# Kernel optimization log

Hardware: AMD Instinct MI355X
Metric: run time of the kernel (lower is better)

## Reference

```python
import jax, jax.numpy as jnp
import numpy as np

N = 100000
E = 1600000
F_IN = 256
H1, C1 = 4, 32          # layer 1: heads=4, out_channels=32, concat=True -> 128
H2, C2 = 1, 16          # layer 2: heads=1, out_channels=nclass=16, concat=False
SLOPE = 0.2             # leaky relu negative slope


def setup_inputs() -> dict:
    key = jax.random.key(0)
    ks = jax.random.split(key, 10)
    x = jax.random.normal(ks[0], (N, F_IN), dtype=jnp.float32)
    row = jax.random.randint(ks[1], (E,), 0, N, dtype=jnp.int32)      # source j
    off = jax.random.randint(ks[2], (E,), 1, N, dtype=jnp.int32)
    col = ((row + off) % N).astype(jnp.int32)                          # target i, no self loops
    edge_index = jnp.stack([row, col])

    def glorot(k, shape, fan_in, fan_out):
        lim = np.sqrt(6.0 / (fan_in + fan_out))
        return jax.random.uniform(k, shape, jnp.float32, -lim, lim)

    W1 = glorot(ks[3], (F_IN, H1 * C1), F_IN, H1 * C1)
    att1 = glorot(ks[4], (1, H1, 2 * C1), H1, 2 * C1)
    b1 = jnp.zeros((H1 * C1,), jnp.float32)
    W2 = glorot(ks[5], (H1 * C1, H2 * C2), H1 * C1, H2 * C2)
    att2 = glorot(ks[6], (1, H2, 2 * C2), H2, 2 * C2)
    b2 = jnp.zeros((C2,), jnp.float32)
    return {"x": x, "edge_index": edge_index, "W1": W1, "att1": att1,
            "b1": b1, "W2": W2, "att2": att2, "b2": b2}


def gcn_norm(edge_index, num_nodes):
    # add_remaining_self_loops + symmetric normalization (GeoLayer.norm)
    loop = jnp.arange(num_nodes, dtype=edge_index.dtype)
    row = jnp.concatenate([edge_index[0], loop])
    col = jnp.concatenate([edge_index[1], loop])
    w = jnp.ones(row.shape[0], jnp.float32)
    deg = jax.ops.segment_sum(w, row, num_segments=num_nodes)
    dinv = jnp.where(deg > 0, jax.lax.rsqrt(deg), 0.0)
    return row, col, dinv[row] * w * dinv[col]


def segment_softmax(alpha, seg, num_segments):
    amax = jax.ops.segment_max(alpha, seg, num_segments=num_segments)
    ex = jnp.exp(alpha - amax[seg])
    denom = jax.ops.segment_sum(ex, seg, num_segments=num_segments)
    return ex / (denom[seg] + 1e-16)


def geo_layer(x, row, col, ew, W, att, b, heads, out_ch, concat):
    n = x.shape[0]
    xt = (x @ W).reshape(n, heads, out_ch)
    x_i = xt[col]                         # [E+N, H, C] target features
    x_j = xt[row]                         # [E+N, H, C] source features
    wl, wr = att[:, :, :out_ch], att[:, :, out_ch:]
    # (cat([x_i,x_j],-1) * att).sum(-1) == (x_i*wl).sum + (x_j*wr).sum
    alpha = (x_i * wl).sum(-1) + (x_j * wr).sum(-1)     # [E+N, H]
    alpha = jnp.where(alpha >= 0, alpha, SLOPE * alpha)  # leaky_relu
    alpha = segment_softmax(alpha, col, n)
    msg = ew[:, None, None] * x_j * alpha[:, :, None]    # [E+N, H, C]
    out = jax.ops.segment_sum(msg, col, num_segments=n)  # scatter-add to targets
    out = out.reshape(n, heads * out_ch) if concat else out.mean(axis=1)
    return out + b


def reference(x, edge_index, W1, att1, b1, W2, att2, b2):
    # norm is identical for both layers (edge_weight=None each time)
    row, col, ew = gcn_norm(edge_index, x.shape[0])
    h = geo_layer(x, row, col, ew, W1, att1, b1, H1, C1, True)
    h = jax.nn.relu(h)
    out = geo_layer(h, row, col, ew, W2, att2, b2, H2, C2, False)
    return out
```

## Files before the change

kernel.cpp:

```cpp
#include <hip/hip_runtime.h>
#include <math.h>

#define TPB 256
#define SEGN 512
#define SCAP 14336
#define CHB 8192
#define CAPC 12288

__device__ __forceinline__ float lrelu(float a){ return a >= 0.f ? a : 0.2f*a; }

typedef __attribute__((ext_vector_type(8))) short bf16x8;
typedef __attribute__((ext_vector_type(4))) float f32x4;

__device__ __forceinline__ unsigned short bfr(float f){
  unsigned u = __float_as_uint(f);
  return (unsigned short)((u + 0x7fffu + ((u >> 16) & 1u)) >> 16);
}

__device__ __forceinline__ void gl_lds16(const void* g, void* l){
  __builtin_amdgcn_global_load_lds(
      (const __attribute__((address_space(1))) void*)g,
      (__attribute__((address_space(3))) void*)l, 16, 0, 0);
}


__global__ __launch_bounds__(256) void k_bucketM(const int* __restrict__ rows, const int* __restrict__ cols,
    int* __restrict__ bcurC, int* __restrict__ bcurR,
    unsigned* __restrict__ ebufC, unsigned short* __restrict__ ebufR, int E, int NSEG2){
  __shared__ int lhC[256], lbC[256], lhR[256], lbR[256];
  int tid = threadIdx.x;
  int e0 = blockIdx.x * CHB;
  #pragma unroll 1
  for(int r=0; r<4; r++){
    lhC[tid] = 0; lhR[tid] = 0;
    __syncthreads();
    int eb = e0 + r*2048;
    unsigned pk[8]; int sgC[8], rkC[8], sgR[8], rkR[8]; int pvR[8];
    #pragma unroll
    for(int i=0;i<8;i++){
      int e = eb + i*256 + tid;
      sgC[i] = -1;
      if(e < E){
        int cc = cols[e], rr = rows[e];
        sgC[i] = cc >> 9;
        pk[i]  = ((unsigned)(cc & (SEGN-1)) << 17) | (unsigned)rr;
        rkC[i] = atomicAdd(&lhC[sgC[i]], 1);
        sgR[i] = rr >> 9;
        pvR[i] = rr & (SEGN-1);
        rkR[i] = atomicAdd(&lhR[sgR[i]], 1);
      }
    }
    __syncthreads();
    if(tid < NSEG2){
      int c = lhC[tid];  lbC[tid] = c  ? atomicAdd(&bcurC[tid], c)  : 0;
      int c2 = lhR[tid]; lbR[tid] = c2 ? atomicAdd(&bcurR[tid], c2) : 0;
    }
    __syncthreads();
    #pragma unroll
    for(int i=0;i<8;i++)
      if(sgC[i] >= 0){
        int p = lbC[sgC[i]] + rkC[i];
        if(p < CAPC) ebufC[sgC[i]*CAPC + p] = pk[i];
        int p2 = lbR[sgR[i]] + rkR[i];
        if(p2 < CAPC) ebufR[sgR[i]*CAPC + p2] = (unsigned short)pvR[i];
      }
    __syncthreads();
  }
}

__global__ __launch_bounds__(256) void k_cntseg(const int* __restrict__ bcurC, const int* __restrict__ bcurR,
    const unsigned* __restrict__ ebufC, const unsigned short* __restrict__ ebufR,
    int* __restrict__ cnt, float* __restrict__ dinv, int* __restrict__ bsum, int N){
  __shared__ int hc[SEGN];
  __shared__ int hr[SEGN];
  __shared__ int red[256];
  int s = blockIdx.x, tid = threadIdx.x;
  int lo = s*SEGN;
  int nn = min(SEGN, N - lo);
  for(int i=tid; i<SEGN; i+=256){ hc[i] = 0; hr[i] = 0; }
  __syncthreads();
  int cb = s*CAPC;
  int cc = min(bcurC[s], CAPC);
  int rc = min(bcurR[s], CAPC);
  for(int j=tid; j<cc; j+=256) atomicAdd(&hc[ebufC[cb + j] >> 17], 1);
  for(int j=tid; j<rc; j+=256) atomicAdd(&hr[ebufR[cb + j]], 1);
  __syncthreads();
  int tsum = 0;
  for(int i=tid; i<nn; i+=256){
    int c = hc[i] + 1;
    cnt[lo+i]  = c;
    tsum += c;
    dinv[lo+i] = 1.f / sqrtf((float)(hr[i] + 1));
  }
  red[tid] = tsum; __syncthreads();
  for(int off=128; off>0; off>>=1){
    if(tid < off) red[tid] += red[tid+off];
    __syncthreads();
  }
  if(tid == 0) bsum[s] = red[0];
}

__global__ void k_scan_bsum(int* bsum, int NB){
  __shared__ int s[256];
  int t = threadIdx.x;
  int v = (t < NB) ? bsum[t] : 0;
  s[t] = v; __syncthreads();
  for(int off=1; off<256; off<<=1){
    int add = (t >= off) ? s[t-off] : 0;
    __syncthreads();
    s[t] += add;
    __syncthreads();
  }
  if(t < NB) bsum[t] = s[t] - v;
}

__global__ __launch_bounds__(256) void k_sortfill2(const int* __restrict__ cnt,
    const int* __restrict__ bsum, const int* __restrict__ bcurC,
    const unsigned* __restrict__ ebuf, int* __restrict__ offs,
    int* __restrict__ csr, int N){
  __shared__ int lcur[SEGN];
  __shared__ int lbuf[SCAP];
  __shared__ int sdata[256];
  int s = blockIdx.x, tid = threadIdx.x;
  int lo = s*SEGN;
  int nn = min(SEGN, N - lo);
  int base = bsum[s];
  int i0 = tid*2, i1 = i0+1;
  int v0 = (i0 < nn) ? cnt[lo+i0] : 0;
  int v1 = (i1 < nn) ? cnt[lo+i1] : 0;
  int ssum = v0 + v1;
  sdata[tid] = ssum; __syncthreads();
  int mine = ssum;
  for(int off=1; off<256; off<<=1){
    int add = (tid >= off) ? sdata[tid-off] : 0;
    __syncthreads();
    sdata[tid] += add;
    __syncthreads();
  }
  int total = sdata[255];
  int run0 = sdata[tid] - mine;
  int run1 = run0 + v0;
  int eb = s*CAPC;
  int ec = min(bcurC[s], CAPC);
  if(total <= SCAP){
    if(i0 < nn){
      offs[lo+i0] = base + run0;
      lbuf[run0]  = lo + i0;
      lcur[i0]    = run0 + 1;
      if(lo+i0 == N-1) offs[N] = base + run0 + v0;
    }
    if(i1 < nn){
      offs[lo+i1] = base + run1;
      lbuf[run1]  = lo + i1;
      lcur[i1]    = run1 + 1;
      if(lo+i1 == N-1) offs[N] = base + run1 + v1;
    }
    __syncthreads();
    for(int j=tid; j<ec; j+=256){
      unsigned pk = ebuf[eb + j];
      int li  = pk >> 17;
      int row = pk & 0x1FFFF;
      int p = atomicAdd(&lcur[li], 1);
      lbuf[p] = row;
    }
    __syncthreads();
    for(int j=tid; j<total; j+=256) csr[base + j] = lbuf[j];
  } else {
    if(i0 < nn){
      offs[lo+i0] = base + run0;
      csr[base+run0] = lo + i0;
      lcur[i0] = base + run0 + 1;
      if(lo+i0 == N-1) offs[N] = base + run0 + v0;
    }
    if(i1 < nn){
      offs[lo+i1] = base + run1;
      csr[base+run1] = lo + i1;
      lcur[i1] = base + run1 + 1;
      if(lo+i1 == N-1) offs[N] = base + run1 + v1;
    }
    __syncthreads();
    for(int j=tid; j<ec; j+=256){
      unsigned pk = ebuf[eb + j];
      int li  = pk >> 17;
      int row = pk & 0x1FFFF;
      int p = atomicAdd(&lcur[li], 1);
      csr[p] = row;
    }
  }
}


__global__ void k_prepW(const float* __restrict__ W, short* __restrict__ Whi,
                        short* __restrict__ Wlo){
  int idx = blockIdx.x*256 + threadIdx.x;
  int n = idx >> 8, k = idx & 255;
  float f = W[k*128 + n];
  unsigned short h = bfr(f);
  float hf = __uint_as_float(((unsigned)h) << 16);
  Whi[n*256 + k] = (short)h;
  Wlo[n*256 + k] = (short)bfr(f - hf);
}


#define BUFB 24576
__global__ __launch_bounds__(256) void k_gemm1(
    const float* __restrict__ x,
    const short* __restrict__ Whi, const short* __restrict__ Wlo,
    const float* __restrict__ att1,
    unsigned* __restrict__ xtb, float* __restrict__ sl, float* __restrict__ sr, int N){
  __shared__ __align__(16) char smem[2*BUFB];
  float* fx = (float*)smem;
  float* att_sh = (float*)(smem + 17408);

  int tid = threadIdx.x;
  int n0 = blockIdx.x * 64;
  int w = tid >> 6, l = tid & 63;
  int wm = w & 1, wn = w >> 1;
  int lm = l & 15, lq = l >> 4;

  f32x4 acc[2][4];
  #pragma unroll
  for(int a=0;a<2;a++)
    #pragma unroll
    for(int b=0;b<4;b++) acc[a][b] = (f32x4){0.f,0.f,0.f,0.f};

  int ua0 = (w<<6) | l, ua1 = 256 + ua0;
  int ar0 = ua0 >> 3, as0 = (ua0 & 7) ^ (ar0 & 7);
  int ar1 = ua1 >> 3, as1 = (ua1 & 7) ^ (ar1 & 7);
  const float* gA0 = x + (size_t)min(n0 + ar0, N-1)*256 + as0*4;
  const float* gA1 = x + (size_t)min(n0 + ar1, N-1)*256 + as1*4;
  int ub0 = (w<<6) | l,  ub1 = 256 + ub0;
  int br0 = ub0 >> 2, bs0 = (ub0 & 3) ^ ((br0 >> 1) & 3);
  int br1 = ub1 >> 2, bs1 = (ub1 & 3) ^ ((br1 >> 1) & 3);
  const short* gBh0 = Whi + br0*256 + bs0*8;
  const short* gBh1 = Whi + br1*256 + bs1*8;
  const short* gBl0 = Wlo + br0*256 + bs0*8;
  const short* gBl1 = Wlo + br1*256 + bs1*8;
  int woff = w << 10;

  int offAf[2][2], offB[4];
  #pragma unroll
  for(int mt=0;mt<2;mt++){
    int rr = wm*32 + mt*16 + lm;
    offAf[mt][0] = rr*32 + (((2*lq+0) ^ (rr&7)) << 2);
    offAf[mt][1] = rr*32 + (((2*lq+1) ^ (rr&7)) << 2);
  }
  #pragma unroll
  for(int nt=0;nt<4;nt++){
    int rr = wn*64 + nt*16 + lm;
    offB[nt] = rr*32 + ((lq ^ ((rr>>1)&3)) << 3);
  }

  {
    char* base = smem;
    gl_lds16(gA0,  base          + woff);
    gl_lds16(gA1,  base + 4096   + woff);
    gl_lds16(gBh0, base + 8192   + woff);
    gl_lds16(gBh1, base + 12288  + woff);
    gl_lds16(gBl0, base + 16384  + woff);
    gl_lds16(gBl1, base + 20480  + woff);
  }
  __syncthreads();

  int cur = 0;
  #pragma unroll 1
  for(int c=0;c<8;c++){
    if(c < 7){
      int kf = (c+1) << 5;
      char* base = smem + (cur^1)*BUFB;
      gl_lds16(gA0  + kf, base          + woff);
      gl_lds16(gA1  + kf, base + 4096   + woff);
      gl_lds16(gBh0 + kf, base + 8192   + woff);
      gl_lds16(gBh1 + kf, base + 12288  + woff);
      gl_lds16(gBl0 + kf, base + 16384  + woff);
      gl_lds16(gBl1 + kf, base + 20480  + woff);
    }
    float* Axf = (float*)(smem + cur*BUFB);
    short* Bh  = (short*)(smem + cur*BUFB + 8192);
    short* Bl  = (short*)(smem + cur*BUFB + 16384);
    bf16x8 ah[2], al2[2];
    #pragma unroll
    for(int mt=0;mt<2;mt++){
      float4 f0 = *((const float4*)&Axf[offAf[mt][0]]);
      float4 f1 = *((const float4*)&Axf[offAf[mt][1]]);
      float fa[8] = {f0.x,f0.y,f0.z,f0.w,f1.x,f1.y,f1.z,f1.w};
      #pragma unroll
      for(int j=0;j<8;j++){
        unsigned short hb = bfr(fa[j]);
        float hf = __uint_as_float(((unsigned)hb) << 16);
        ah[mt][j]  = (short)hb;
        al2[mt][j] = (short)bfr(fa[j] - hf);
      }
    }
    #pragma unroll
    for(int nt=0;nt<4;nt++){
      bf16x8 bh = *((bf16x8*)&Bh[offB[nt]]);
      bf16x8 bl = *((bf16x8*)&Bl[offB[nt]]);
      #pragma unroll
      for(int mt=0;mt<2;mt++){
        acc[mt][nt] = __builtin_amdgcn_mfma_f32_16x16x32_bf16(ah[mt],  bh, acc[mt][nt], 0,0,0);
        acc[mt][nt] = __builtin_amdgcn_mfma_f32_16x16x32_bf16(ah[mt],  bl, acc[mt][nt], 0,0,0);
        acc[mt][nt] = __builtin_amdgcn_mfma_f32_16x16x32_bf16(al2[mt], bh, acc[mt][nt], 0,0,0);
      }
    }
    __syncthreads();
    cur ^= 1;
  }

  #pragma unroll
  for(int mt=0;mt<2;mt++){
    #pragma unroll
    for(int v=0;v<4;v++){
      int row = n0 + wm*32 + mt*16 + lq*4 + v;
      if(row < N){
        unsigned p0 = (unsigned)bfr(acc[mt][0][v]) | ((unsigned)bfr(acc[mt][2][v])<<16);
        unsigned p1 = (unsigned)bfr(acc[mt][1][v]) | ((unsigned)bfr(acc[mt][3][v])<<16);
        int jb = wn*32 + lm;
        xtb[(size_t)row*64 + jb]      = p0;
        xtb[(size_t)row*64 + jb + 16] = p1;
      }
    }
  }

  att_sh[tid] = att1[tid];
  #pragma unroll 1
  for(int p=0;p<2;p++){
    __syncthreads();
    if(wn == p){
      #pragma unroll
      for(int mt=0;mt<2;mt++)
        #pragma unroll
        for(int nt=0;nt<4;nt++)
          #pragma unroll
          for(int v=0;v<4;v++)
            fx[(wm*32 + mt*16 + lq*4 + v)*68 + nt*16 + lm] = acc[mt][nt][v];
    }
    __syncthreads();
    if(tid < 128){
      int rloc = tid >> 1, hh = tid & 1;
      int head = p*2 + hh;
      float a = 0.f, b = 0.f;
      #pragma unroll
      for(int c4=0;c4<8;c4++){
        float4 xv  = *((const float4*)&fx[rloc*68 + hh*32 + c4*4]);
        float4 alv = *((const float4*)&att_sh[head*64 + c4*4]);
        float4 arv = *((const float4*)&att_sh[head*64 + 32 + c4*4]);
        a += xv.x*alv.x + xv.y*alv.y + xv.z*alv.z + xv.w*alv.w;
        b += xv.x*arv.x + xv.y*arv.y + xv.z*arv.z + xv.w*arv.w;
      }
      int row = n0 + rloc;
      if(row < N){
        sl[(size_t)row*4 + head] = a;
        sr[(size_t)row*4 + head] = b;
      }
    }
  }
}


__global__ __launch_bounds__(64) void k_agg1(const int* __restrict__ offs, const int* __restrict__ srcs,
    const float* __restrict__ sl, const float* __restrict__ sr, const float* __restrict__ dinv,
    const unsigned* __restrict__ xtb, const float* __restrict__ b1, float* __restrict__ h, int N){
  __shared__ int   s_sh[64];
  __shared__ float w_sh[64*4];
  int n = blockIdx.x;
  if(n >= N) return;
  int lane = threadIdx.x;
  int beg = offs[n], end = offs[n+1];
  int deg = end - beg;
  float4 sln = *((const float4*)(sl + (size_t)n*4));
  int h0 = lane >> 5;
  float den0=0.f,den1=0.f,den2=0.f,den3=0.f;
  float acc0=0.f, acc1=0.f;

  if(deg <= 64){
    int j = beg + lane;
    int s = 0; float wd = 0.f;
    float a0=-1e30f, a1=-1e30f, a2=-1e30f, a3=-1e30f;
    if(j < end){
      s = srcs[j];
      float4 a = *((const float4*)(sr + (size_t)s*4));
      a0 = lrelu(sln.x + a.x);
      a1 = lrelu(sln.y + a.y);
      a2 = lrelu(sln.z + a.z);
      a3 = lrelu(sln.w + a.w);
      wd = dinv[s];
    }
    float m0=a0,m1=a1,m2=a2,m3=a3;
    #pragma unroll
    for(int o=32;o>0;o>>=1){
      m0 = fmaxf(m0, __shfl_xor(m0,o));
      m1 = fmaxf(m1, __shfl_xor(m1,o));
      m2 = fmaxf(m2, __shfl_xor(m2,o));
      m3 = fmaxf(m3, __shfl_xor(m3,o));
    }
    den0 = __expf(a0 - m0);
    den1 = __expf(a1 - m1);
    den2 = __expf(a2 - m2);
    den3 = __expf(a3 - m3);
    s_sh[lane] = s;
    w_sh[lane*4+0] = wd*den0;
    w_sh[lane*4+1] = wd*den1;
    w_sh[lane*4+2] = wd*den2;
    w_sh[lane*4+3] = wd*den3;
    __syncthreads();
    int k = 0;
    for(; k+8<=deg; k+=8){
      int sk[8];
      #pragma unroll
      for(int u=0;u<8;u++) sk[u] = __builtin_amdgcn_readfirstlane(s_sh[k+u]);
      unsigned pv[8];
      #pragma unroll
      for(int u=0;u<8;u++) pv[u] = xtb[(size_t)sk[u]*64 + lane];
      #pragma unroll
      for(int u=0;u<8;u++){
        float2 wv = *((const float2*)&w_sh[(k+u)*4 + h0*2]);
        acc0 += wv.x * __uint_as_float(pv[u] << 16);
        acc1 += wv.y * __uint_as_float(pv[u] & 0xffff0000u);
      }
    }
    for(; k<deg; k++){
      int sk = __builtin_amdgcn_readfirstlane(s_sh[k]);
      unsigned pvv = xtb[(size_t)sk*64 + lane];
      float2 wv = *((const float2*)&w_sh[k*4 + h0*2]);
      acc0 += wv.x * __uint_as_float(pvv << 16);
      acc1 += wv.y * __uint_as_float(pvv & 0xffff0000u);
    }
  } else {
    float m0=-1e30f,m1=-1e30f,m2=-1e30f,m3=-1e30f;
    for(int j=beg+lane; j<end; j+=64){
      int s = srcs[j];
      float4 a = *((const float4*)(sr + (size_t)s*4));
      m0 = fmaxf(m0, lrelu(sln.x + a.x));
      m1 = fmaxf(m1, lrelu(sln.y + a.y));
      m2 = fmaxf(m2, lrelu(sln.z + a.z));
      m3 = fmaxf(m3, lrelu(sln.w + a.w));
    }
    #pragma unroll
    for(int o=32;o>0;o>>=1){
      m0 = fmaxf(m0, __shfl_xor(m0,o));
      m1 = fmaxf(m1, __shfl_xor(m1,o));
      m2 = fmaxf(m2, __shfl_xor(m2,o));
      m3 = fmaxf(m3, __shfl_xor(m3,o));
    }
    for(int c0=beg; c0<end; c0+=64){
      int cnt = min(64, end-c0);
      int j = c0 + lane;
      float e0=0.f,e1=0.f,e2=0.f,e3=0.f, wd=0.f; int s=0;
      if(j<end){
        s = srcs[j];
        float4 a = *((const float4*)(sr + (size_t)s*4));
        e0 = __expf(lrelu(sln.x + a.x) - m0);
        e1 = __expf(lrelu(sln.y + a.y) - m1);
        e2 = __expf(lrelu(sln.z + a.z) - m2);
        e3 = __expf(lrelu(sln.w + a.w) - m3);
        wd = dinv[s];
      }
      den0+=e0; den1+=e1; den2+=e2; den3+=e3;
      s_sh[lane] = s;
      w_sh[lane*4+0] = wd*e0;
      w_sh[lane*4+1] = wd*e1;
      w_sh[lane*4+2] = wd*e2;
      w_sh[lane*4+3] = wd*e3;
      __syncthreads();
      int k = 0;
      for(; k+8<=cnt; k+=8){
        int sk[8];
        #pragma unroll
        for(int u=0;u<8;u++) sk[u] = __builtin_amdgcn_readfirstlane(s_sh[k+u]);
        unsigned pv[8];
        #pragma unroll
        for(int u=0;u<8;u++) pv[u] = xtb[(size_t)sk[u]*64 + lane];
        #pragma unroll
        for(int u=0;u<8;u++){
          float2 wv = *((const float2*)&w_sh[(k+u)*4 + h0*2]);
          acc0 += wv.x * __uint_as_float(pv[u] << 16);
          acc1 += wv.y * __uint_as_float(pv[u] & 0xffff0000u);
        }
      }
      for(; k<cnt; k++){
        int sk = __builtin_amdgcn_readfirstlane(s_sh[k]);
        unsigned pvv = xtb[(size_t)sk*64 + lane];
        float2 wv = *((const float2*)&w_sh[k*4 + h0*2]);
        acc0 += wv.x * __uint_as_float(pvv << 16);
        acc1 += wv.y * __uint_as_float(pvv & 0xffff0000u);
      }
      __syncthreads();
    }
  }
  #pragma unroll
  for(int o=32;o>0;o>>=1){
    den0 += __shfl_xor(den0,o);
    den1 += __shfl_xor(den1,o);
    den2 += __shfl_xor(den2,o);
    den3 += __shfl_xor(den3,o);
  }
  float din = dinv[n];
  int ch0 = (lane < 32) ? lane : lane + 32;
  int ch1 = ch0 + 32;
  float d0 = (lane < 32) ? den0 : den2;
  float d1 = (lane < 32) ? den1 : den3;
  float o0 = din*acc0/(d0 + 1e-16f) + b1[ch0];
  float o1 = din*acc1/(d1 + 1e-16f) + b1[ch1];
  h[(size_t)n*128 + ch0] = o0 > 0.f ? o0 : 0.f;
  h[(size_t)n*128 + ch1] = o1 > 0.f ? o1 : 0.f;
}


__global__ __launch_bounds__(256) void k_gemm2(const float* __restrict__ hmat, const float* __restrict__ W2,
    const float* __restrict__ att2, unsigned* __restrict__ xt2b,
    float* __restrict__ sl2, float* __restrict__ sr2, int N){
  __shared__ float hs[16*132];
  __shared__ float ws[16*132];
  __shared__ float xs[16*16];
  int t = threadIdx.x;
  int n0 = blockIdx.x * 16;
  #pragma unroll
  for(int i=0;i<8;i++){
    int idx = t + 256*i;
    int k = idx >> 4, c = idx & 15;
    ws[c*132 + k] = W2[idx];
  }
  #pragma unroll
  for(int i=0;i<2;i++){
    int idx = t + 256*i;
    int r = idx >> 5, k4 = idx & 31;
    int n = n0 + r;
    float4 v = make_float4(0.f,0.f,0.f,0.f);
    if(n < N) v = ((const float4*)hmat)[(size_t)n*32 + k4];
    *((float4*)&hs[r*132 + k4*4]) = v;
  }
  __syncthreads();
  int r = t >> 4, c = t & 15;
  float acc = 0.f;
  for(int k=0;k<128;k+=4){
    float4 hv = *((const float4*)&hs[r*132+k]);
    float4 wv = *((const float4*)&ws[c*132+k]);
    acc += hv.x*wv.x + hv.y*wv.y + hv.z*wv.z + hv.w*wv.w;
  }
  xs[r*16 + c] = acc;
  __syncthreads();
  int n = n0 + r;
  if(c < 8 && n < N){
    unsigned pk = (unsigned)bfr(xs[r*16+c]) | ((unsigned)bfr(xs[r*16+c+8])<<16);
    xt2b[(size_t)n*8 + c] = pk;
  }
  if(t < 16){
    int nn = n0 + t;
    if(nn < N){
      float a = 0.f, b = 0.f;
      #pragma unroll
      for(int cc=0;cc<16;cc++){ float v = xs[t*16+cc]; a += v*att2[cc]; b += v*att2[16+cc]; }
      sl2[nn] = a; sr2[nn] = b;
    }
  }
}


__global__ __launch_bounds__(64) void k_agg2(const int* __restrict__ offs, const int* __restrict__ srcs,
    const float* __restrict__ sl2, const float* __restrict__ sr2, const float* __restrict__ dinv,
    const unsigned* __restrict__ xt2b, const float* __restrict__ b2, float* __restrict__ out, int N){
  __shared__ int   s_sh[64];
  __shared__ float w_sh[64];
  int n = blockIdx.x;
  if(n >= N) return;
  int lane = threadIdx.x;
  int beg = offs[n], end = offs[n+1];
  int deg = end - beg;
  float sln = sl2[n];
  float den = 0.f, acc0 = 0.f, acc1 = 0.f;
  int grp = lane >> 3, ch = lane & 7;

  if(deg <= 64){
    int j = beg + lane;
    int s = 0; float wd = 0.f; float a = -1e30f;
    if(j < end){
      s = srcs[j];
      a = lrelu(sln + sr2[s]);
      wd = dinv[s];
    }
    float m = a;
    #pragma unroll
    for(int o=32;o>0;o>>=1) m = fmaxf(m, __shfl_xor(m,o));
    float e = __expf(a - m);
    den = e;
    s_sh[lane] = s;
    w_sh[lane] = wd*e;
    __syncthreads();
    for(int k=0;k<deg;k+=8){
      int kk = k + grp;
      if(kk < deg){
        int sk = s_sh[kk];
        float wk = w_sh[kk];
        unsigned pv = xt2b[(size_t)sk*8 + ch];
        acc0 += wk * __uint_as_float(pv << 16);
        acc1 += wk * __uint_as_float(pv & 0xffff0000u);
      }
    }
  } else {
    float m = -1e30f;
    for(int j=beg+lane; j<end; j+=64)
      m = fmaxf(m, lrelu(sln + sr2[srcs[j]]));
    #pragma unroll
    for(int o=32;o>0;o>>=1) m = fmaxf(m, __shfl_xor(m,o));
    for(int c0=beg; c0<end; c0+=64){
      int cnt = min(64, end-c0);
      int j = c0 + lane;
      float e=0.f, wd=0.f; int s=0;
      if(j<end){
        s = srcs[j];
        e = __expf(lrelu(sln + sr2[s]) - m);
        wd = dinv[s];
      }
      den += e;
      s_sh[lane] = s;
      w_sh[lane] = wd*e;
      __syncthreads();
      for(int k=0;k<cnt;k+=8){
        int kk = k + grp;
        if(kk < cnt){
          int sk = s_sh[kk];
          float wk = w_sh[kk];
          unsigned pv = xt2b[(size_t)sk*8 + ch];
          acc0 += wk * __uint_as_float(pv << 16);
          acc1 += wk * __uint_as_float(pv & 0xffff0000u);
        }
      }
      __syncthreads();
    }
  }
  #pragma unroll
  for(int o=32;o>0;o>>=1) den += __shfl_xor(den,o);
  acc0 += __shfl_xor(acc0,8);  acc0 += __shfl_xor(acc0,16);  acc0 += __shfl_xor(acc0,32);
  acc1 += __shfl_xor(acc1,8);  acc1 += __shfl_xor(acc1,16);  acc1 += __shfl_xor(acc1,32);
  if(lane < 8){
    float din = dinv[n];
    out[(size_t)n*16 + lane]     = din*acc0/(den + 1e-16f) + b2[lane];
    out[(size_t)n*16 + lane + 8] = din*acc1/(den + 1e-16f) + b2[lane+8];
  }
}


extern "C" void kernel_launch(void* const* d_in, const int* in_sizes, int n_in,
                              void* d_out, int out_size, void* d_ws, size_t ws_size,
                              hipStream_t stream){
  const float* x    = (const float*)d_in[0];
  const int*   ei   = (const int*)d_in[1];
  const float* W1   = (const float*)d_in[2];
  const float* att1 = (const float*)d_in[3];
  const float* b1   = (const float*)d_in[4];
  const float* W2   = (const float*)d_in[5];
  const float* att2 = (const float*)d_in[6];
  const float* b2   = (const float*)d_in[7];
  int N = in_sizes[0] / 256;
  int E = in_sizes[1] / 2;
  const int* rows = ei;
  const int* cols = ei + E;
  float* out = (float*)d_out;

  int ET    = E + N;
  int NSEG2 = (N + SEGN - 1) / SEGN;

  char* p = (char*)d_ws;
  auto alloc = [&](size_t bytes)->void*{ void* q = p; p += (bytes + 255) & ~(size_t)255; return q; };
  int*      cnt     = (int*)alloc((size_t)N*4);
  int*      offs    = (int*)alloc((size_t)(N+1)*4);
  int*      bsum    = (int*)alloc(256*4);
  int*      bcur    = (int*)alloc(512*4);
  int*      csr     = (int*)alloc((size_t)ET*4);
  float*    dinv    = (float*)alloc((size_t)N*4);
  unsigned* xtb     = (unsigned*)alloc((size_t)N*64*4);
  float*    sl1     = (float*)alloc((size_t)N*16);
  float*    sr1     = (float*)alloc((size_t)N*16);
  float*    hbuf    = (float*)alloc((size_t)N*128*4);
  unsigned* xt2b    = (unsigned*)alloc((size_t)N*8*4);
  float*    sl2     = (float*)alloc((size_t)N*4);
  float*    sr2     = (float*)alloc((size_t)N*4);
  short*    Whi     = (short*)alloc((size_t)128*256*2);
  short*    Wlo     = (short*)alloc((size_t)128*256*2);

  int* bcurC = bcur;
  int* bcurR = bcur + 256;

  unsigned*       ebufC = (unsigned*)xtb;
  unsigned short* ebufR = (unsigned short*)(ebufC + (size_t)NSEG2*CAPC);

  int gB = (E + CHB - 1) / CHB;

  hipMemsetAsync(bcur, 0, 512*4, stream);
  k_bucketM<<<gB, 256, 0, stream>>>(rows, cols, bcurC, bcurR, ebufC, ebufR, E, NSEG2);
  k_cntseg<<<NSEG2, 256, 0, stream>>>(bcurC, bcurR, ebufC, ebufR, cnt, dinv, bsum, N);
  k_scan_bsum<<<1, 256, 0, stream>>>(bsum, NSEG2);
  k_sortfill2<<<NSEG2, 256, 0, stream>>>(cnt, bsum, bcurC, ebufC, offs, csr, N);

  k_prepW<<<128, 256, 0, stream>>>(W1, Whi, Wlo);
  k_gemm1<<<(N + 63)/64, 256, 0, stream>>>(x, Whi, Wlo, att1, xtb, sl1, sr1, N);
  k_agg1<<<N, 64, 0, stream>>>(offs, csr, sl1, sr1, dinv, xtb, b1, hbuf, N);

  k_gemm2<<<(N + 15)/16, 256, 0, stream>>>(hbuf, W2, att2, xt2b, sl2, sr2, N);
  k_agg2<<<N, 64, 0, stream>>>(offs, csr, sl2, sr2, dinv, xt2b, b2, out, N);
}
```

Before: 406.4 us.

## Fuse edge bucketing into GEMM1 launch and merge CSR build kernels

Edge bucketing blocks and the layer-1 GEMM blocks now run inside one launch, with block index selecting the role, so the bucketing can overlap the GEMM. The degree count, block-sum scan and CSR fill kernels are merged into a single per-segment kernel, and each block recomputes the global prefix over segment totals itself. This cuts several kernel launches and the intermediate cnt/bsum buffers. In exchange the edge buffers need their own workspace allocation instead of aliasing xtb, and the single merged kernel does a redundant scan in every block.

```diff
diff --git a/kernel.cpp b/kernel.cpp
--- a/kernel.cpp
+++ b/kernel.cpp
@@ -21,172 +21,6 @@
   __builtin_amdgcn_global_load_lds(
       (const __attribute__((address_space(1))) void*)g,
       (__attribute__((address_space(3))) void*)l, 16, 0, 0);
-}
-
-
-__global__ __launch_bounds__(256) void k_bucketM(const int* __restrict__ rows, const int* __restrict__ cols,
-    int* __restrict__ bcurC, int* __restrict__ bcurR,
-    unsigned* __restrict__ ebufC, unsigned short* __restrict__ ebufR, int E, int NSEG2){
-  __shared__ int lhC[256], lbC[256], lhR[256], lbR[256];
-  int tid = threadIdx.x;
-  int e0 = blockIdx.x * CHB;
-  #pragma unroll 1
-  for(int r=0; r<4; r++){
-    lhC[tid] = 0; lhR[tid] = 0;
-    __syncthreads();
-    int eb = e0 + r*2048;
-    unsigned pk[8]; int sgC[8], rkC[8], sgR[8], rkR[8]; int pvR[8];
-    #pragma unroll
-    for(int i=0;i<8;i++){
-      int e = eb + i*256 + tid;
-      sgC[i] = -1;
-      if(e < E){
-        int cc = cols[e], rr = rows[e];
-        sgC[i] = cc >> 9;
-        pk[i]  = ((unsigned)(cc & (SEGN-1)) << 17) | (unsigned)rr;
-        rkC[i] = atomicAdd(&lhC[sgC[i]], 1);
-        sgR[i] = rr >> 9;
-        pvR[i] = rr & (SEGN-1);
-        rkR[i] = atomicAdd(&lhR[sgR[i]], 1);
-      }
-    }
-    __syncthreads();
-    if(tid < NSEG2){
-      int c = lhC[tid];  lbC[tid] = c  ? atomicAdd(&bcurC[tid], c)  : 0;
-      int c2 = lhR[tid]; lbR[tid] = c2 ? atomicAdd(&bcurR[tid], c2) : 0;
-    }
-    __syncthreads();
-    #pragma unroll
-    for(int i=0;i<8;i++)
-      if(sgC[i] >= 0){
-        int p = lbC[sgC[i]] + rkC[i];
-        if(p < CAPC) ebufC[sgC[i]*CAPC + p] = pk[i];
-        int p2 = lbR[sgR[i]] + rkR[i];
-        if(p2 < CAPC) ebufR[sgR[i]*CAPC + p2] = (unsigned short)pvR[i];
-      }
-    __syncthreads();
-  }
-}
-
-__global__ __launch_bounds__(256) void k_cntseg(const int* __restrict__ bcurC, const int* __restrict__ bcurR,
-    const unsigned* __restrict__ ebufC, const unsigned short* __restrict__ ebufR,
-    int* __restrict__ cnt, float* __restrict__ dinv, int* __restrict__ bsum, int N){
-  __shared__ int hc[SEGN];
-  __shared__ int hr[SEGN];
-  __shared__ int red[256];
-  int s = blockIdx.x, tid = threadIdx.x;
-  int lo = s*SEGN;
-  int nn = min(SEGN, N - lo);
-  for(int i=tid; i<SEGN; i+=256){ hc[i] = 0; hr[i] = 0; }
-  __syncthreads();
-  int cb = s*CAPC;
-  int cc = min(bcurC[s], CAPC);
-  int rc = min(bcurR[s], CAPC);
-  for(int j=tid; j<cc; j+=256) atomicAdd(&hc[ebufC[cb + j] >> 17], 1);
-  for(int j=tid; j<rc; j+=256) atomicAdd(&hr[ebufR[cb + j]], 1);
-  __syncthreads();
-  int tsum = 0;
-  for(int i=tid; i<nn; i+=256){
-    int c = hc[i] + 1;
-    cnt[lo+i]  = c;
-    tsum += c;
-    dinv[lo+i] = 1.f / sqrtf((float)(hr[i] + 1));
-  }
-  red[tid] = tsum; __syncthreads();
-  for(int off=128; off>0; off>>=1){
-    if(tid < off) red[tid] += red[tid+off];
-    __syncthreads();
-  }
-  if(tid == 0) bsum[s] = red[0];
-}
-
-__global__ void k_scan_bsum(int* bsum, int NB){
-  __shared__ int s[256];
-  int t = threadIdx.x;
-  int v = (t < NB) ? bsum[t] : 0;
-  s[t] = v; __syncthreads();
-  for(int off=1; off<256; off<<=1){
-    int add = (t >= off) ? s[t-off] : 0;
-    __syncthreads();
-    s[t] += add;
-    __syncthreads();
-  }
-  if(t < NB) bsum[t] = s[t] - v;
-}
-
-__global__ __launch_bounds__(256) void k_sortfill2(const int* __restrict__ cnt,
-    const int* __restrict__ bsum, const int* __restrict__ bcurC,
-    const unsigned* __restrict__ ebuf, int* __restrict__ offs,
-    int* __restrict__ csr, int N){
-  __shared__ int lcur[SEGN];
-  __shared__ int lbuf[SCAP];
-  __shared__ int sdata[256];
-  int s = blockIdx.x, tid = threadIdx.x;
-  int lo = s*SEGN;
-  int nn = min(SEGN, N - lo);
-  int base = bsum[s];
-  int i0 = tid*2, i1 = i0+1;
-  int v0 = (i0 < nn) ? cnt[lo+i0] : 0;
-  int v1 = (i1 < nn) ? cnt[lo+i1] : 0;
-  int ssum = v0 + v1;
-  sdata[tid] = ssum; __syncthreads();
-  int mine = ssum;
-  for(int off=1; off<256; off<<=1){
-    int add = (tid >= off) ? sdata[tid-off] : 0;
-    __syncthreads();
-    sdata[tid] += add;
-    __syncthreads();
-  }
-  int total = sdata[255];
-  int run0 = sdata[tid] - mine;
-  int run1 = run0 + v0;
-  int eb = s*CAPC;
-  int ec = min(bcurC[s], CAPC);
-  if(total <= SCAP){
-    if(i0 < nn){
-      offs[lo+i0] = base + run0;
-      lbuf[run0]  = lo + i0;
-      lcur[i0]    = run0 + 1;
-      if(lo+i0 == N-1) offs[N] = base + run0 + v0;
-    }
-    if(i1 < nn){
-      offs[lo+i1] = base + run1;
-      lbuf[run1]  = lo + i1;
-      lcur[i1]    = run1 + 1;
-      if(lo+i1 == N-1) offs[N] = base + run1 + v1;
-    }
-    __syncthreads();
-    for(int j=tid; j<ec; j+=256){
-      unsigned pk = ebuf[eb + j];
-      int li  = pk >> 17;
-      int row = pk & 0x1FFFF;
-      int p = atomicAdd(&lcur[li], 1);
-      lbuf[p] = row;
-    }
-    __syncthreads();
-    for(int j=tid; j<total; j+=256) csr[base + j] = lbuf[j];
-  } else {
-    if(i0 < nn){
-      offs[lo+i0] = base + run0;
-      csr[base+run0] = lo + i0;
-      lcur[i0] = base + run0 + 1;
-      if(lo+i0 == N-1) offs[N] = base + run0 + v0;
-    }
-    if(i1 < nn){
-      offs[lo+i1] = base + run1;
-      csr[base+run1] = lo + i1;
-      lcur[i1] = base + run1 + 1;
-      if(lo+i1 == N-1) offs[N] = base + run1 + v1;
-    }
-    __syncthreads();
-    for(int j=tid; j<ec; j+=256){
-      unsigned pk = ebuf[eb + j];
-      int li  = pk >> 17;
-      int row = pk & 0x1FFFF;
-      int p = atomicAdd(&lcur[li], 1);
-      csr[p] = row;
-    }
-  }
 }
 
 
@@ -203,17 +37,69 @@
 
 
 #define BUFB 24576
-__global__ __launch_bounds__(256) void k_gemm1(
+__global__ __launch_bounds__(256) void k_mega1(
+    const int* __restrict__ rows, const int* __restrict__ cols,
+    int* __restrict__ bcurC, int* __restrict__ bcurR,
+    unsigned* __restrict__ ebufC, unsigned short* __restrict__ ebufR,
+    int E, int NSEG2, int gB,
     const float* __restrict__ x,
     const short* __restrict__ Whi, const short* __restrict__ Wlo,
     const float* __restrict__ att1,
     unsigned* __restrict__ xtb, float* __restrict__ sl, float* __restrict__ sr, int N){
   __shared__ __align__(16) char smem[2*BUFB];
+
+  if(blockIdx.x < gB){
+    int* lhC = (int*)smem;
+    int* lbC = (int*)(smem + 1024);
+    int* lhR = (int*)(smem + 2048);
+    int* lbR = (int*)(smem + 3072);
+    int tid = threadIdx.x;
+    int e0 = blockIdx.x * CHB;
+    #pragma unroll 1
+    for(int r=0; r<4; r++){
+      lhC[tid] = 0; lhR[tid] = 0;
+      __syncthreads();
+      int eb = e0 + r*2048;
+      unsigned pk[8]; int sgC[8], rkC[8], sgR[8], rkR[8]; int pvR[8];
+      #pragma unroll
+      for(int i=0;i<8;i++){
+        int e = eb + i*256 + tid;
+        sgC[i] = -1;
+        if(e < E){
+          int cc = cols[e], rr = rows[e];
+          sgC[i] = cc >> 9;
+          pk[i]  = ((unsigned)(cc & (SEGN-1)) << 17) | (unsigned)rr;
+          rkC[i] = atomicAdd(&lhC[sgC[i]], 1);
+          sgR[i] = rr >> 9;
+          pvR[i] = rr & (SEGN-1);
+          rkR[i] = atomicAdd(&lhR[sgR[i]], 1);
+        }
+      }
+      __syncthreads();
+      if(tid < NSEG2){
+        int c = lhC[tid];  lbC[tid] = c  ? atomicAdd(&bcurC[tid], c)  : 0;
+        int c2 = lhR[tid]; lbR[tid] = c2 ? atomicAdd(&bcurR[tid], c2) : 0;
+      }
+      __syncthreads();
+      #pragma unroll
+      for(int i=0;i<8;i++)
+        if(sgC[i] >= 0){
+          int p = lbC[sgC[i]] + rkC[i];
+          if(p < CAPC) ebufC[sgC[i]*CAPC + p] = pk[i];
+          int p2 = lbR[sgR[i]] + rkR[i];
+          if(p2 < CAPC) ebufR[sgR[i]*CAPC + p2] = (unsigned short)pvR[i];
+        }
+      __syncthreads();
+    }
+    return;
+  }
+
+  int bid = blockIdx.x - gB;
   float* fx = (float*)smem;
   float* att_sh = (float*)(smem + 17408);
 
   int tid = threadIdx.x;
-  int n0 = blockIdx.x * 64;
+  int n0 = bid * 64;
   int w = tid >> 6, l = tid & 63;
   int wm = w & 1, wn = w >> 1;
   int lm = l & 15, lq = l >> 4;
@@ -353,6 +239,109 @@
         sl[(size_t)row*4 + head] = a;
         sr[(size_t)row*4 + head] = b;
       }
+    }
+  }
+}
+
+
+__global__ __launch_bounds__(256) void k_buildseg(const int* __restrict__ bcurC,
+    const int* __restrict__ bcurR,
+    const unsigned* __restrict__ ebufC, const unsigned short* __restrict__ ebufR,
+    float* __restrict__ dinv, int* __restrict__ offs, int* __restrict__ csr,
+    int N, int NSEG2){
+  __shared__ int hc[SEGN];
+  __shared__ int hr[SEGN];
+  __shared__ int lcur[SEGN];
+  __shared__ int sdata[256];
+  __shared__ int stot[256];
+  __shared__ int lbuf[SCAP];
+  int s = blockIdx.x, tid = threadIdx.x;
+  int lo = s*SEGN;
+  int nn = min(SEGN, N - lo);
+
+  int tot = 0;
+  if(tid < NSEG2){
+    int nn2 = min(SEGN, N - tid*SEGN);
+    tot = min(bcurC[tid], CAPC) + nn2;
+  }
+  stot[tid] = tot; __syncthreads();
+  for(int off=1; off<256; off<<=1){
+    int add = (tid >= off) ? stot[tid-off] : 0;
+    __syncthreads();
+    stot[tid] += add;
+    __syncthreads();
+  }
+  int cc = min(bcurC[s], CAPC);
+  int base = stot[s] - (cc + nn);
+
+  for(int i=tid; i<SEGN; i+=256){ hc[i] = 0; hr[i] = 0; }
+  __syncthreads();
+  int cb = s*CAPC;
+  int rc = min(bcurR[s], CAPC);
+  for(int j=tid; j<cc; j+=256) atomicAdd(&hc[ebufC[cb + j] >> 17], 1);
+  for(int j=tid; j<rc; j+=256) atomicAdd(&hr[ebufR[cb + j]], 1);
+  __syncthreads();
+  for(int i=tid; i<nn; i+=256) dinv[lo+i] = 1.f / sqrtf((float)(hr[i] + 1));
+
+  int i0 = tid*2, i1 = i0+1;
+  int v0 = (i0 < nn) ? hc[i0] + 1 : 0;
+  int v1 = (i1 < nn) ? hc[i1] + 1 : 0;
+  int ssum = v0 + v1;
+  sdata[tid] = ssum; __syncthreads();
+  int mine = ssum;
+  for(int off=1; off<256; off<<=1){
+    int add = (tid >= off) ? sdata[tid-off] : 0;
+    __syncthreads();
+    sdata[tid] += add;
+    __syncthreads();
+  }
+  int total = sdata[255];
+  int run0 = sdata[tid] - mine;
+  int run1 = run0 + v0;
+
+  if(total <= SCAP){
+    if(i0 < nn){
+      offs[lo+i0] = base + run0;
+      lbuf[run0]  = lo + i0;
+      lcur[i0]    = run0 + 1;
+      if(lo+i0 == N-1) offs[N] = base + run0 + v0;
+    }
+    if(i1 < nn){
+      offs[lo+i1] = base + run1;
+      lbuf[run1]  = lo + i1;
+      lcur[i1]    = run1 + 1;
+      if(lo+i1 == N-1) offs[N] = base + run1 + v1;
+    }
+    __syncthreads();
+    for(int j=tid; j<cc; j+=256){
+      unsigned pk = ebufC[cb + j];
+      int li  = pk >> 17;
+      int row = pk & 0x1FFFF;
+      int p = atomicAdd(&lcur[li], 1);
+      lbuf[p] = row;
+    }
+    __syncthreads();
+    for(int j=tid; j<total; j+=256) csr[base + j] = lbuf[j];
+  } else {
+    if(i0 < nn){
+      offs[lo+i0] = base + run0;
+      csr[base+run0] = lo + i0;
+      lcur[i0] = base + run0 + 1;
+      if(lo+i0 == N-1) offs[N] = base + run0 + v0;
+    }
+    if(i1 < nn){
+      offs[lo+i1] = base + run1;
+      csr[base+run1] = lo + i1;
+      lcur[i1] = base + run1 + 1;
+      if(lo+i1 == N-1) offs[N] = base + run1 + v1;
+    }
+    __syncthreads();
+    for(int j=tid; j<cc; j+=256){
+      unsigned pk = ebufC[cb + j];
+      int li  = pk >> 17;
+      int row = pk & 0x1FFFF;
+      int p = atomicAdd(&lcur[li], 1);
+      csr[p] = row;
     }
   }
 }
@@ -663,9 +652,7 @@
 
   char* p = (char*)d_ws;
   auto alloc = [&](size_t bytes)->void*{ void* q = p; p += (bytes + 255) & ~(size_t)255; return q; };
-  int*      cnt     = (int*)alloc((size_t)N*4);
   int*      offs    = (int*)alloc((size_t)(N+1)*4);
-  int*      bsum    = (int*)alloc(256*4);
   int*      bcur    = (int*)alloc(512*4);
   int*      csr     = (int*)alloc((size_t)ET*4);
   float*    dinv    = (float*)alloc((size_t)N*4);
@@ -678,25 +665,22 @@
   float*    sr2     = (float*)alloc((size_t)N*4);
   short*    Whi     = (short*)alloc((size_t)128*256*2);
   short*    Wlo     = (short*)alloc((size_t)128*256*2);
+  unsigned*       ebufC = (unsigned*)alloc((size_t)NSEG2*CAPC*4);
+  unsigned short* ebufR = (unsigned short*)alloc((size_t)NSEG2*CAPC*2);
 
   int* bcurC = bcur;
   int* bcurR = bcur + 256;
 
-  unsigned*       ebufC = (unsigned*)xtb;
-  unsigned short* ebufR = (unsigned short*)(ebufC + (size_t)NSEG2*CAPC);
-
   int gB = (E + CHB - 1) / CHB;
+  int gG = (N + 63) / 64;
 
   hipMemsetAsync(bcur, 0, 512*4, stream);
-  k_bucketM<<<gB, 256, 0, stream>>>(rows, cols, bcurC, bcurR, ebufC, ebufR, E, NSEG2);
-  k_cntseg<<<NSEG2, 256, 0, stream>>>(bcurC, bcurR, ebufC, ebufR, cnt, dinv, bsum, N);
-  k_scan_bsum<<<1, 256, 0, stream>>>(bsum, NSEG2);
-  k_sortfill2<<<NSEG2, 256, 0, stream>>>(cnt, bsum, bcurC, ebufC, offs, csr, N);
-
   k_prepW<<<128, 256, 0, stream>>>(W1, Whi, Wlo);
-  k_gemm1<<<(N + 63)/64, 256, 0, stream>>>(x, Whi, Wlo, att1, xtb, sl1, sr1, N);
+  k_mega1<<<gB + gG, 256, 0, stream>>>(rows, cols, bcurC, bcurR, ebufC, ebufR,
+                                       E, NSEG2, gB,
+                                       x, Whi, Wlo, att1, xtb, sl1, sr1, N);
+  k_buildseg<<<NSEG2, 256, 0, stream>>>(bcurC, bcurR, ebufC, ebufR, dinv, offs, csr, N, NSEG2);
   k_agg1<<<N, 64, 0, stream>>>(offs, csr, sl1, sr1, dinv, xtb, b1, hbuf, N);
-
   k_gemm2<<<(N + 15)/16, 256, 0, stream>>>(hbuf, W2, att2, xt2b, sl2, sr2, N);
   k_agg2<<<N, 64, 0, stream>>>(offs, csr, sl2, sr2, dinv, xt2b, b2, out, N);
 }
```

Result: faster. 379.9 us (-6.5%).
